# Performance work log

Measured on AMD Instinct MI355X. Metric: run time of the kernel, lower is better.

Reference implementation:

```python
import jax, jax.numpy as jnp
import numpy as np

N, E, F_IN, HID, HEADS, CLASSES = 50000, 800000, 128, 128, 4, 2
NEG_SLOPE = 0.2


def _gatv2_layer(x, Wl, Wr, att, bias, src, dst, heads, concat):
    # PyG GATv2Conv (share_weights=False, eval mode):
    #   e_ij = att . leaky_relu(Wl x_j + Wr x_i); alpha = segment_softmax over dst;
    #   out_i = sum_j alpha_ij * (Wl x_j)
    n = x.shape[0]
    c = att.shape[-1]
    xl = (x @ Wl).reshape(n, heads, c)   # source transform [N,H,C]
    xr = (x @ Wr).reshape(n, heads, c)   # target transform [N,H,C]
    e = jax.nn.leaky_relu(xl[src] + xr[dst], NEG_SLOPE)      # [E,H,C]
    logits = jnp.einsum('ehc,hc->eh', e, att)                # [E,H]
    m = jax.ops.segment_max(logits, dst, num_segments=n)     # stable softmax per dst
    p = jnp.exp(logits - m[dst])
    denom = jax.ops.segment_sum(p, dst, num_segments=n)
    alpha = p / (denom[dst] + 1e-16)                         # [E,H]
    out = jax.ops.segment_sum(alpha[:, :, None] * xl[src], dst, num_segments=n)  # [N,H,C]
    out = out.reshape(n, heads * c) if concat else out.mean(axis=1)
    return out + bias


def setup_inputs() -> dict:
    key = jax.random.key(0)
    ks = jax.random.split(key, 16)
    s = lambda fan_in: 1.0 / np.sqrt(fan_in)
    inp = {
        'x': jax.random.normal(ks[0], (N, F_IN), jnp.float32),
        'edge_idx': jax.random.randint(ks[1], (2, E), 0, N, jnp.int64),
        'w_in': jax.random.normal(ks[2], (F_IN, HID), jnp.float32) * s(F_IN),
        'b_in': jnp.zeros((HID,), jnp.float32),
        'wl1': jax.random.normal(ks[3], (HID, HEADS * HID), jnp.float32) * s(HID),
        'wr1': jax.random.normal(ks[4], (HID, HEADS * HID), jnp.float32) * s(HID),
        'att1': jax.random.normal(ks[5], (HEADS, HID), jnp.float32) * s(HID),
        'b1': jnp.zeros((HEADS * HID,), jnp.float32),
        'wl2': jax.random.normal(ks[6], (HEADS * HID, HID), jnp.float32) * s(HEADS * HID),
        'wr2': jax.random.normal(ks[7], (HEADS * HID, HID), jnp.float32) * s(HEADS * HID),
        'att2': jax.random.normal(ks[8], (1, HID), jnp.float32) * s(HID),
        'b2': jnp.zeros((HID,), jnp.float32),
        'w_out': jax.random.normal(ks[9], (HID, CLASSES), jnp.float32) * s(HID),
        'b_out': jnp.zeros((CLASSES,), jnp.float32),
    }
    return inp


def reference(x, edge_idx, w_in, b_in, wl1, wr1, att1, b1, wl2, wr2, att2, b2, w_out, b_out):
    n = x.shape[0]
    loops = jnp.arange(n, dtype=edge_idx.dtype)  # PyG add_self_loops=True
    src = jnp.concatenate([edge_idx[0], loops])
    dst = jnp.concatenate([edge_idx[1], loops])
    h = jax.nn.elu(x @ w_in + b_in)              # dropout is identity in eval
    h = jax.nn.elu(_gatv2_layer(h, wl1, wr1, att1, b1, src, dst, HEADS, True))
    h = jax.nn.elu(_gatv2_layer(h, wl2, wr2, att2, b2, src, dst, 1, False))
    logits = h @ w_out + b_out
    return jax.nn.log_softmax(logits, axis=1)
```

## Files before the change

kernel.cpp:

```cpp
#include <hip/hip_runtime.h>
#include <hip/hip_bf16.h>
#include <math.h>

#define F_IN   128
#define HID    128
#define HEADS  4
#define HC1    (HEADS*HID)
#define CLASSES 2
#define NEG_SLOPE 0.2f

#define SCAN_CHUNK 2048

typedef __attribute__((ext_vector_type(8))) short short8;
typedef __attribute__((ext_vector_type(4))) float f32x4;

__global__ void zero_int_kernel(int* __restrict__ p, int n) {
    int i = blockIdx.x * blockDim.x + threadIdx.x;
    int stride = gridDim.x * blockDim.x;
    for (; i < n; i += stride) p[i] = 0;
}

__global__ void deg_kernel(const int* __restrict__ dst_arr, int* __restrict__ deg,
                           int E, int N) {
    int e = blockIdx.x * blockDim.x + threadIdx.x;
    if (e >= E) return;
    int d = dst_arr[e];
    if ((unsigned)d >= (unsigned)N) d = 0;
    atomicAdd(&deg[d], 1);
}

__global__ void scan_partial_kernel(const int* __restrict__ deg, int* __restrict__ bsum, int n) {
    __shared__ int sdata[256];
    int b = blockIdx.x, t = threadIdx.x;
    int base = b * SCAN_CHUNK;
    int s = 0;
    for (int i = t; i < SCAN_CHUNK; i += 256) {
        int idx = base + i;
        s += (idx < n) ? deg[idx] : 0;
    }
    sdata[t] = s;
    __syncthreads();
    for (int off = 128; off; off >>= 1) {
        if (t < off) sdata[t] += sdata[t + off];
        __syncthreads();
    }
    if (t == 0) bsum[b] = sdata[0];
}

__global__ void scan_bsums_kernel(int* __restrict__ bsum, int nb, int* __restrict__ row, int n) {
    if (blockIdx.x == 0 && threadIdx.x == 0) {
        int acc = 0;
        for (int i = 0; i < nb; ++i) { int v = bsum[i]; bsum[i] = acc; acc += v; }
        row[n] = acc;
    }
}

__global__ void scan_final_kernel(const int* __restrict__ deg, const int* __restrict__ bsum,
                                  int* __restrict__ row, int* __restrict__ cursor, int n) {
    __shared__ int tsum[256];
    int b = blockIdx.x, t = threadIdx.x;
    int base = b * SCAN_CHUNK + t * 8;
    int local[8];
    int s = 0;
    #pragma unroll
    for (int k = 0; k < 8; ++k) {
        int idx = base + k;
        int v = (idx < n) ? deg[idx] : 0;
        local[k] = s;
        s += v;
    }
    tsum[t] = s;
    __syncthreads();
    for (int off = 1; off < 256; off <<= 1) {
        int v = 0;
        if (t >= off) v = tsum[t - off];
        __syncthreads();
        if (t >= off) tsum[t] += v;
        __syncthreads();
    }
    int texcl = (t == 0) ? 0 : tsum[t - 1];
    int boff = bsum[b];
    #pragma unroll
    for (int k = 0; k < 8; ++k) {
        int idx = base + k;
        if (idx < n) {
            int v = boff + texcl + local[k];
            row[idx] = v;
            cursor[idx] = v;
        }
    }
}

__global__ void scatter_kernel(const int* __restrict__ src_arr, const int* __restrict__ dst_arr,
                               int* __restrict__ cursor, int* __restrict__ src_sorted,
                               int E, int N) {
    int e = blockIdx.x * blockDim.x + threadIdx.x;
    if (e >= E) return;
    int s = src_arr[e], d = dst_arr[e];
    if ((unsigned)s >= (unsigned)N) s = 0;
    if ((unsigned)d >= (unsigned)N) d = 0;
    int pos = atomicAdd(&cursor[d], 1);
    src_sorted[pos] = s;
}

__global__ void transpose_to_bf16_kernel(const float* __restrict__ w,
                                         __hip_bfloat16* __restrict__ wT,
                                         int K, int N) {
    int t = blockIdx.x * blockDim.x + threadIdx.x;
    if (t >= K * N) return;
    int n = t / K, k = t % K;
    wT[t] = __float2bfloat16(w[(size_t)k * N + n]);
}

__global__ void f32_to_bf16_kernel(const float* __restrict__ in,
                                   __hip_bfloat16* __restrict__ outb, int n) {
    int i = blockIdx.x * blockDim.x + threadIdx.x;
    int stride = gridDim.x * blockDim.x;
    short* ob = (short*)outb;
    for (int base = i * 4; base < n; base += stride * 4) {
        float4 v = *(const float4*)(in + base);
        __hip_bfloat16 h0 = __float2bfloat16(v.x);
        __hip_bfloat16 h1 = __float2bfloat16(v.y);
        __hip_bfloat16 h2 = __float2bfloat16(v.z);
        __hip_bfloat16 h3 = __float2bfloat16(v.w);
        short4 sv;
        sv.x = *reinterpret_cast<short*>(&h0);
        sv.y = *reinterpret_cast<short*>(&h1);
        sv.z = *reinterpret_cast<short*>(&h2);
        sv.w = *reinterpret_cast<short*>(&h3);
        *(short4*)(ob + base) = sv;
    }
}

template<int ACT, typename OutT>
__global__ __launch_bounds__(256) void gemm_kernel(
    const float* __restrict__ A, const float* __restrict__ B,
    const float* __restrict__ bias, OutT* __restrict__ C,
    int M, int K, int N)
{
    const int tx = threadIdx.x & 15;
    const int ty = threadIdx.x >> 4;
    const int row0 = blockIdx.y * 64;
    const int col0 = blockIdx.x * 64;

    __shared__ float As[16][68];
    __shared__ float Bs[16][68];

    float acc[4][4] = {};

    for (int k0 = 0; k0 < K; k0 += 16) {
        #pragma unroll
        for (int idx = threadIdx.x; idx < 64 * 16; idx += 256) {
            int r = idx >> 4, c = idx & 15;
            int gr = row0 + r;
            float v = (gr < M) ? A[(size_t)gr * K + (k0 + c)] : 0.0f;
            As[c][r] = v;
        }
        #pragma unroll
        for (int idx = threadIdx.x; idx < 16 * 64; idx += 256) {
            int r = idx >> 6, c = idx & 63;
            Bs[r][c] = B[(size_t)(k0 + r) * N + (col0 + c)];
        }
        __syncthreads();
        #pragma unroll
        for (int k = 0; k < 16; ++k) {
            float a[4], b[4];
            #pragma unroll
            for (int i = 0; i < 4; ++i) a[i] = As[k][ty * 4 + i];
            #pragma unroll
            for (int j = 0; j < 4; ++j) b[j] = Bs[k][tx * 4 + j];
            #pragma unroll
            for (int i = 0; i < 4; ++i)
                #pragma unroll
                for (int j = 0; j < 4; ++j)
                    acc[i][j] += a[i] * b[j];
        }
        __syncthreads();
    }

    #pragma unroll
    for (int i = 0; i < 4; ++i) {
        int r = row0 + ty * 4 + i;
        if (r >= M) continue;
        #pragma unroll
        for (int j = 0; j < 4; ++j) {
            int c = col0 + tx * 4 + j;
            float v = acc[i][j] + (bias ? bias[c] : 0.0f);
            if (ACT == 1) v = (v > 0.0f) ? v : expm1f(v);
            C[(size_t)r * N + c] = (OutT)v;
        }
    }
}

template<typename OutT>
__global__ __launch_bounds__(256) void mfma_gemm_kernel(
    const __hip_bfloat16* __restrict__ A,
    const __hip_bfloat16* __restrict__ BT,
    OutT* __restrict__ C,
    int M, int K, int N)
{
    constexpr int BM = 128, BN = 64, BK = 64, LDA = 72;
    __shared__ __align__(16) short As[BM * LDA];
    __shared__ __align__(16) short Bs[BN * LDA];

    const int tid  = threadIdx.x;
    const int lane = tid & 63;
    const int wid  = tid >> 6;
    const int wm   = wid >> 1;
    const int wn   = wid & 1;
    const int fr   = lane & 15;
    const int fk   = (lane >> 4) * 8;

    const int row0 = blockIdx.y * BM;
    const int col0 = blockIdx.x * BN;

    const short* Ag = (const short*)A;
    const short* Bg = (const short*)BT;

    f32x4 acc[4][2] = {};

    for (int k0 = 0; k0 < K; k0 += BK) {
        #pragma unroll
        for (int it = 0; it < 4; ++it) {
            int chunk = it * 256 + tid;
            int r = chunk >> 3, c = chunk & 7;
            int gr = row0 + r;
            short8 v = {0, 0, 0, 0, 0, 0, 0, 0};
            if (gr < M) v = *(const short8*)(Ag + (size_t)gr * K + k0 + c * 8);
            *(short8*)(&As[r * LDA + c * 8]) = v;
        }
        #pragma unroll
        for (int it = 0; it < 2; ++it) {
            int chunk = it * 256 + tid;
            int n = chunk >> 3, c = chunk & 7;
            short8 v = *(const short8*)(Bg + (size_t)(col0 + n) * K + k0 + c * 8);
            *(short8*)(&Bs[n * LDA + c * 8]) = v;
        }
        __syncthreads();
        #pragma unroll
        for (int kk = 0; kk < 2; ++kk) {
            short8 af[4], bf[2];
            #pragma unroll
            for (int i = 0; i < 4; ++i)
                af[i] = *(const short8*)(&As[(wm * 64 + i * 16 + fr) * LDA + kk * 32 + fk]);
            #pragma unroll
            for (int j = 0; j < 2; ++j)
                bf[j] = *(const short8*)(&Bs[(wn * 32 + j * 16 + fr) * LDA + kk * 32 + fk]);
            #pragma unroll
            for (int i = 0; i < 4; ++i)
                #pragma unroll
                for (int j = 0; j < 2; ++j)
                    acc[i][j] = __builtin_amdgcn_mfma_f32_16x16x32_bf16(af[i], bf[j], acc[i][j], 0, 0, 0);
        }
        __syncthreads();
    }

    const int crow = row0 + wm * 64;
    const int ccol = col0 + wn * 32;
    #pragma unroll
    for (int i = 0; i < 4; ++i) {
        #pragma unroll
        for (int j = 0; j < 2; ++j) {
            int col = ccol + j * 16 + (lane & 15);
            #pragma unroll
            for (int reg = 0; reg < 4; ++reg) {
                int r = crow + i * 16 + (lane >> 4) * 4 + reg;
                if (r < M) C[(size_t)r * N + col] = (OutT)acc[i][j][reg];
            }
        }
    }
}

__global__ __launch_bounds__(256) void gatv2_l1_fused_kernel(
    const __hip_bfloat16* __restrict__ xl, const __hip_bfloat16* __restrict__ xr,
    const int* __restrict__ row, const int* __restrict__ src_sorted,
    const float* __restrict__ att, const float* __restrict__ b1,
    __hip_bfloat16* __restrict__ out1, int N)
{
    int d = blockIdx.x * 4 + (threadIdx.x >> 6);
    if (d >= N) return;
    int lane = threadIdx.x & 63;
    int cbase = lane * 8;

    float xrd[8], attv[8];
    {
        uint4 raw = *reinterpret_cast<const uint4*>(xr + (size_t)d * HC1 + cbase);
        const unsigned* u = reinterpret_cast<const unsigned*>(&raw);
        #pragma unroll
        for (int j = 0; j < 4; ++j) {
            xrd[2 * j]     = __uint_as_float(u[j] << 16);
            xrd[2 * j + 1] = __uint_as_float(u[j] & 0xffff0000u);
        }
        #pragma unroll
        for (int k = 0; k < 8; ++k) attv[k] = att[cbase + k];
    }

    float m = -__builtin_huge_valf();
    float s = 0.0f;
    float o[8] = {};

    int rs = row[d], re = row[d + 1];

    for (int it = rs - 1; it < re; ++it) {
        int srcn = (it < rs) ? d : src_sorted[it];
        float v[8];
        uint4 raw = *reinterpret_cast<const uint4*>(xl + (size_t)srcn * HC1 + cbase);
        const unsigned* u = reinterpret_cast<const unsigned*>(&raw);
        #pragma unroll
        for (int j = 0; j < 4; ++j) {
            v[2 * j]     = __uint_as_float(u[j] << 16);
            v[2 * j + 1] = __uint_as_float(u[j] & 0xffff0000u);
        }
        float t = 0.0f;
        #pragma unroll
        for (int k = 0; k < 8; ++k) {
            float e = v[k] + xrd[k];
            e = (e > 0.0f) ? e : NEG_SLOPE * e;
            t = fmaf(e, attv[k], t);
        }
        t += __shfl_xor(t, 1);
        t += __shfl_xor(t, 2);
        t += __shfl_xor(t, 4);
        t += __shfl_xor(t, 8);
        if (t > m) {
            float r = __expf(m - t);
            s *= r;
            #pragma unroll
            for (int k = 0; k < 8; ++k) o[k] *= r;
            m = t;
        }
        float p = __expf(t - m);
        s += p;
        #pragma unroll
        for (int k = 0; k < 8; ++k) o[k] = fmaf(p, v[k], o[k]);
    }

    float inv = 1.0f / (s + 1e-16f);
    short8 sv;
    #pragma unroll
    for (int k = 0; k < 8; ++k) {
        float val = o[k] * inv + b1[cbase + k];
        val = (val > 0.0f) ? val : expm1f(val);
        __hip_bfloat16 hb = __float2bfloat16(val);
        sv[k] = *reinterpret_cast<short*>(&hb);
    }
    *(short8*)((short*)out1 + (size_t)d * HC1 + cbase) = sv;
}

__global__ __launch_bounds__(256) void gatv2_l2_final_kernel(
    const float* __restrict__ xl2, const float* __restrict__ xr2,
    const int* __restrict__ row, const int* __restrict__ src_sorted,
    const float* __restrict__ att2, const float* __restrict__ b2,
    const float* __restrict__ w_out, const float* __restrict__ b_out,
    float* __restrict__ out, int N)
{
    int d = blockIdx.x * 4 + (threadIdx.x >> 6);
    if (d >= N) return;
    int lane = threadIdx.x & 63;
    int c0 = lane * 2;

    float2 xrd  = *reinterpret_cast<const float2*>(xr2 + (size_t)d * HID + c0);
    float2 attv = *reinterpret_cast<const float2*>(att2 + c0);

    float m = -__builtin_huge_valf();
    float s = 0.0f;
    float o0 = 0.0f, o1 = 0.0f;

    int rs = row[d], re = row[d + 1];
    for (int it = rs - 1; it < re; ++it) {
        int srcn = (it < rs) ? d : src_sorted[it];
        float2 v = *reinterpret_cast<const float2*>(xl2 + (size_t)srcn * HID + c0);
        float e0 = v.x + xrd.x; e0 = (e0 > 0.0f) ? e0 : NEG_SLOPE * e0;
        float e1 = v.y + xrd.y; e1 = (e1 > 0.0f) ? e1 : NEG_SLOPE * e1;
        float t = fmaf(e0, attv.x, e1 * attv.y);
        #pragma unroll
        for (int off = 32; off; off >>= 1) t += __shfl_xor(t, off);
        if (t > m) {
            float r = __expf(m - t);
            s *= r; o0 *= r; o1 *= r;
            m = t;
        }
        float p = __expf(t - m);
        s += p;
        o0 = fmaf(p, v.x, o0);
        o1 = fmaf(p, v.y, o1);
    }

    float inv = 1.0f / (s + 1e-16f);
    float h0v = o0 * inv + b2[c0];
    float h1v = o1 * inv + b2[c0 + 1];
    h0v = (h0v > 0.0f) ? h0v : expm1f(h0v);
    h1v = (h1v > 0.0f) ? h1v : expm1f(h1v);

    float a0 = fmaf(h0v, w_out[c0 * 2 + 0], h1v * w_out[(c0 + 1) * 2 + 0]);
    float a1 = fmaf(h0v, w_out[c0 * 2 + 1], h1v * w_out[(c0 + 1) * 2 + 1]);
    #pragma unroll
    for (int off = 32; off; off >>= 1) {
        a0 += __shfl_xor(a0, off);
        a1 += __shfl_xor(a1, off);
    }
    if (lane == 0) {
        float z0 = a0 + b_out[0];
        float z1 = a1 + b_out[1];
        float mx = fmaxf(z0, z1);
        float lse = mx + logf(__expf(z0 - mx) + __expf(z1 - mx));
        out[(size_t)d * CLASSES + 0] = z0 - lse;
        out[(size_t)d * CLASSES + 1] = z1 - lse;
    }
}

extern "C" void kernel_launch(void* const* d_in, const int* in_sizes, int n_in,
                              void* d_out, int out_size, void* d_ws, size_t ws_size,
                              hipStream_t stream)
{
    const float* x     = (const float*)d_in[0];
    const int*   eidx  = (const int*)d_in[1];
    const float* w_in  = (const float*)d_in[2];
    const float* b_in  = (const float*)d_in[3];
    const float* wl1   = (const float*)d_in[4];
    const float* wr1   = (const float*)d_in[5];
    const float* att1  = (const float*)d_in[6];
    const float* b1    = (const float*)d_in[7];
    const float* wl2   = (const float*)d_in[8];
    const float* wr2   = (const float*)d_in[9];
    const float* att2  = (const float*)d_in[10];
    const float* b2    = (const float*)d_in[11];
    const float* w_out = (const float*)d_in[12];
    const float* b_out = (const float*)d_in[13];
    float* out = (float*)d_out;

    const int N = in_sizes[0] / F_IN;
    const int E = in_sizes[1] / 2;
    const int* src_arr = eidx;
    const int* dst_arr = eidx + E;

    size_t off = 0;
    auto alloc = [&](size_t bytes) -> char* {
        char* ptr = (char*)d_ws + off;
        off += (bytes + 255) & ~(size_t)255;
        return ptr;
    };
    int* row        = (int*)alloc((size_t)(N + 1) * 4);
    int* cursor     = (int*)alloc((size_t)N * 4);
    int* deg        = (int*)alloc((size_t)N * 4);
    int* bsum       = (int*)alloc(64 * 4);
    int* src_sorted = (int*)alloc((size_t)E * 4);
    __hip_bfloat16* wT1l = (__hip_bfloat16*)alloc((size_t)HID * HC1 * 2);
    __hip_bfloat16* wT1r = (__hip_bfloat16*)alloc((size_t)HID * HC1 * 2);
    __hip_bfloat16* wT2l = (__hip_bfloat16*)alloc((size_t)HC1 * HID * 2);
    __hip_bfloat16* wT2r = (__hip_bfloat16*)alloc((size_t)HC1 * HID * 2);
    float*          h0   = (float*)alloc((size_t)N * HID * 4);
    __hip_bfloat16* h0b  = (__hip_bfloat16*)alloc((size_t)N * HID * 2);
    __hip_bfloat16* xl1  = (__hip_bfloat16*)alloc((size_t)N * HC1 * 2);
    __hip_bfloat16* xr1  = (__hip_bfloat16*)alloc((size_t)N * HC1 * 2);
    __hip_bfloat16* out1 = (__hip_bfloat16*)alloc((size_t)N * HC1 * 2);

    float* xl2 = h0;
    float* xr2 = (float*)xl1;

    dim3 blk(256);
    const int NB_SCAN = (N + SCAN_CHUNK - 1) / SCAN_CHUNK;

    hipLaunchKernelGGL(zero_int_kernel, dim3(64), blk, 0, stream, deg, N);
    hipLaunchKernelGGL(deg_kernel, dim3((E + 255) / 256), blk, 0, stream, dst_arr, deg, E, N);
    hipLaunchKernelGGL(scan_partial_kernel, dim3(NB_SCAN), blk, 0, stream, deg, bsum, N);
    hipLaunchKernelGGL(scan_bsums_kernel, dim3(1), blk, 0, stream, bsum, NB_SCAN, row, N);
    hipLaunchKernelGGL(scan_final_kernel, dim3(NB_SCAN), blk, 0, stream, deg, bsum, row, cursor, N);
    hipLaunchKernelGGL(scatter_kernel, dim3((E + 255) / 256), blk, 0, stream,
                       src_arr, dst_arr, cursor, src_sorted, E, N);

    {
        dim3 gw((HID * HC1 + 255) / 256);
        hipLaunchKernelGGL(transpose_to_bf16_kernel, gw, blk, 0, stream, wl1, wT1l, HID, HC1);
        hipLaunchKernelGGL(transpose_to_bf16_kernel, gw, blk, 0, stream, wr1, wT1r, HID, HC1);
        hipLaunchKernelGGL(transpose_to_bf16_kernel, gw, blk, 0, stream, wl2, wT2l, HC1, HID);
        hipLaunchKernelGGL(transpose_to_bf16_kernel, gw, blk, 0, stream, wr2, wT2r, HC1, HID);
    }

    {
        dim3 grid(HID / 64, (N + 63) / 64);
        hipLaunchKernelGGL((gemm_kernel<1, float>), grid, blk, 0, stream,
                           x, w_in, b_in, h0, N, F_IN, HID);
        hipLaunchKernelGGL(f32_to_bf16_kernel, dim3(2048), blk, 0, stream, h0, h0b, N * HID);
    }
    {
        dim3 grid(HC1 / 64, (N + 127) / 128);
        hipLaunchKernelGGL((mfma_gemm_kernel<__hip_bfloat16>), grid, blk, 0, stream,
                           h0b, wT1l, xl1, N, HID, HC1);
        hipLaunchKernelGGL((mfma_gemm_kernel<__hip_bfloat16>), grid, blk, 0, stream,
                           h0b, wT1r, xr1, N, HID, HC1);
    }
    {
        dim3 grid((N + 3) / 4);
        hipLaunchKernelGGL(gatv2_l1_fused_kernel, grid, blk, 0, stream,
                           xl1, xr1, row, src_sorted, att1, b1, out1, N);
    }
    {
        dim3 grid(HID / 64, (N + 127) / 128);
        hipLaunchKernelGGL((mfma_gemm_kernel<float>), grid, blk, 0, stream,
                           out1, wT2l, xl2, N, HC1, HID);
        hipLaunchKernelGGL((mfma_gemm_kernel<float>), grid, blk, 0, stream,
                           out1, wT2r, xr2, N, HC1, HID);
    }
    {
        dim3 grid((N + 3) / 4);
        hipLaunchKernelGGL(gatv2_l2_final_kernel, grid, blk, 0, stream,
                           xl2, xr2, row, src_sorted, att2, b2, w_out, b_out, out, N);
    }
}
```

Before: 647.2 us.

## Merge Wl/Wr GEMMs into one, use MFMA for input layer, prefetch gathers

Concatenates the left and right weight matrices so each GAT layer needs a single MFMA GEMM writing an interleaved [xl|xr] bf16 row per node. The input projection moves from the scalar fp32 GEMM to the bf16 MFMA GEMM with fused bias and ELU, and layer-2 features are stored in bf16 instead of fp32, halving gather traffic. Both attention kernels software-prefetch the next neighbour's row to hide gather latency. The cost is lower precision in the input layer and the layer-2 features, and a wider row stride for the gathers.

```diff
diff --git a/kernel.cpp b/kernel.cpp
--- a/kernel.cpp
+++ b/kernel.cpp
@@ -133,69 +133,10 @@
 }
 
 template<int ACT, typename OutT>
-__global__ __launch_bounds__(256) void gemm_kernel(
-    const float* __restrict__ A, const float* __restrict__ B,
-    const float* __restrict__ bias, OutT* __restrict__ C,
-    int M, int K, int N)
-{
-    const int tx = threadIdx.x & 15;
-    const int ty = threadIdx.x >> 4;
-    const int row0 = blockIdx.y * 64;
-    const int col0 = blockIdx.x * 64;
-
-    __shared__ float As[16][68];
-    __shared__ float Bs[16][68];
-
-    float acc[4][4] = {};
-
-    for (int k0 = 0; k0 < K; k0 += 16) {
-        #pragma unroll
-        for (int idx = threadIdx.x; idx < 64 * 16; idx += 256) {
-            int r = idx >> 4, c = idx & 15;
-            int gr = row0 + r;
-            float v = (gr < M) ? A[(size_t)gr * K + (k0 + c)] : 0.0f;
-            As[c][r] = v;
-        }
-        #pragma unroll
-        for (int idx = threadIdx.x; idx < 16 * 64; idx += 256) {
-            int r = idx >> 6, c = idx & 63;
-            Bs[r][c] = B[(size_t)(k0 + r) * N + (col0 + c)];
-        }
-        __syncthreads();
-        #pragma unroll
-        for (int k = 0; k < 16; ++k) {
-            float a[4], b[4];
-            #pragma unroll
-            for (int i = 0; i < 4; ++i) a[i] = As[k][ty * 4 + i];
-            #pragma unroll
-            for (int j = 0; j < 4; ++j) b[j] = Bs[k][tx * 4 + j];
-            #pragma unroll
-            for (int i = 0; i < 4; ++i)
-                #pragma unroll
-                for (int j = 0; j < 4; ++j)
-                    acc[i][j] += a[i] * b[j];
-        }
-        __syncthreads();
-    }
-
-    #pragma unroll
-    for (int i = 0; i < 4; ++i) {
-        int r = row0 + ty * 4 + i;
-        if (r >= M) continue;
-        #pragma unroll
-        for (int j = 0; j < 4; ++j) {
-            int c = col0 + tx * 4 + j;
-            float v = acc[i][j] + (bias ? bias[c] : 0.0f);
-            if (ACT == 1) v = (v > 0.0f) ? v : expm1f(v);
-            C[(size_t)r * N + c] = (OutT)v;
-        }
-    }
-}
-
-template<typename OutT>
 __global__ __launch_bounds__(256) void mfma_gemm_kernel(
     const __hip_bfloat16* __restrict__ A,
     const __hip_bfloat16* __restrict__ BT,
+    const float* __restrict__ bias,
     OutT* __restrict__ C,
     int M, int K, int N)
 {
@@ -262,17 +203,22 @@
         #pragma unroll
         for (int j = 0; j < 2; ++j) {
             int col = ccol + j * 16 + (lane & 15);
+            float bv = bias ? bias[col] : 0.0f;
             #pragma unroll
             for (int reg = 0; reg < 4; ++reg) {
                 int r = crow + i * 16 + (lane >> 4) * 4 + reg;
-                if (r < M) C[(size_t)r * N + col] = (OutT)acc[i][j][reg];
+                if (r < M) {
+                    float v = acc[i][j][reg] + bv;
+                    if (ACT == 1) v = (v > 0.0f) ? v : expm1f(v);
+                    C[(size_t)r * N + col] = (OutT)v;
+                }
             }
         }
     }
 }
 
 __global__ __launch_bounds__(256) void gatv2_l1_fused_kernel(
-    const __hip_bfloat16* __restrict__ xl, const __hip_bfloat16* __restrict__ xr,
+    const __hip_bfloat16* __restrict__ xlr,
     const int* __restrict__ row, const int* __restrict__ src_sorted,
     const float* __restrict__ att, const float* __restrict__ b1,
     __hip_bfloat16* __restrict__ out1, int N)
@@ -281,10 +227,11 @@
     if (d >= N) return;
     int lane = threadIdx.x & 63;
     int cbase = lane * 8;
+    const short* base = (const short*)xlr;
 
     float xrd[8], attv[8];
     {
-        uint4 raw = *reinterpret_cast<const uint4*>(xr + (size_t)d * HC1 + cbase);
+        uint4 raw = *reinterpret_cast<const uint4*>(base + (size_t)d * 1024 + 512 + cbase);
         const unsigned* u = reinterpret_cast<const unsigned*>(&raw);
         #pragma unroll
         for (int j = 0; j < 4; ++j) {
@@ -301,11 +248,15 @@
 
     int rs = row[d], re = row[d + 1];
 
+    uint4 raw = *reinterpret_cast<const uint4*>(base + (size_t)d * 1024 + cbase);
     for (int it = rs - 1; it < re; ++it) {
-        int srcn = (it < rs) ? d : src_sorted[it];
+        uint4 cur = raw;
+        if (it + 1 < re) {
+            int sn = src_sorted[it + 1];
+            raw = *reinterpret_cast<const uint4*>(base + (size_t)sn * 1024 + cbase);
+        }
         float v[8];
-        uint4 raw = *reinterpret_cast<const uint4*>(xl + (size_t)srcn * HC1 + cbase);
-        const unsigned* u = reinterpret_cast<const unsigned*>(&raw);
+        const unsigned* u = reinterpret_cast<const unsigned*>(&cur);
         #pragma unroll
         for (int j = 0; j < 4; ++j) {
             v[2 * j]     = __uint_as_float(u[j] << 16);
@@ -348,7 +299,7 @@
 }
 
 __global__ __launch_bounds__(256) void gatv2_l2_final_kernel(
-    const float* __restrict__ xl2, const float* __restrict__ xr2,
+    const __hip_bfloat16* __restrict__ xlr2,
     const int* __restrict__ row, const int* __restrict__ src_sorted,
     const float* __restrict__ att2, const float* __restrict__ b2,
     const float* __restrict__ w_out, const float* __restrict__ b_out,
@@ -358,8 +309,11 @@
     if (d >= N) return;
     int lane = threadIdx.x & 63;
     int c0 = lane * 2;
-
-    float2 xrd  = *reinterpret_cast<const float2*>(xr2 + (size_t)d * HID + c0);
+    const short* base = (const short*)xlr2;
+
+    unsigned xr_raw = *reinterpret_cast<const unsigned*>(base + (size_t)d * 256 + 128 + c0);
+    float xrd0 = __uint_as_float(xr_raw << 16);
+    float xrd1 = __uint_as_float(xr_raw & 0xffff0000u);
     float2 attv = *reinterpret_cast<const float2*>(att2 + c0);
 
     float m = -__builtin_huge_valf();
@@ -367,11 +321,17 @@
     float o0 = 0.0f, o1 = 0.0f;
 
     int rs = row[d], re = row[d + 1];
+    unsigned raw = *reinterpret_cast<const unsigned*>(base + (size_t)d * 256 + c0);
     for (int it = rs - 1; it < re; ++it) {
-        int srcn = (it < rs) ? d : src_sorted[it];
-        float2 v = *reinterpret_cast<const float2*>(xl2 + (size_t)srcn * HID + c0);
-        float e0 = v.x + xrd.x; e0 = (e0 > 0.0f) ? e0 : NEG_SLOPE * e0;
-        float e1 = v.y + xrd.y; e1 = (e1 > 0.0f) ? e1 : NEG_SLOPE * e1;
+        unsigned cur = raw;
+        if (it + 1 < re) {
+            int sn = src_sorted[it + 1];
+            raw = *reinterpret_cast<const unsigned*>(base + (size_t)sn * 256 + c0);
+        }
+        float v0 = __uint_as_float(cur << 16);
+        float v1 = __uint_as_float(cur & 0xffff0000u);
+        float e0 = v0 + xrd0; e0 = (e0 > 0.0f) ? e0 : NEG_SLOPE * e0;
+        float e1 = v1 + xrd1; e1 = (e1 > 0.0f) ? e1 : NEG_SLOPE * e1;
         float t = fmaf(e0, attv.x, e1 * attv.y);
         #pragma unroll
         for (int off = 32; off; off >>= 1) t += __shfl_xor(t, off);
@@ -382,8 +342,8 @@
         }
         float p = __expf(t - m);
         s += p;
-        o0 = fmaf(p, v.x, o0);
-        o1 = fmaf(p, v.y, o1);
+        o0 = fmaf(p, v0, o0);
+        o1 = fmaf(p, v1, o1);
     }
 
     float inv = 1.0f / (s + 1e-16f);
@@ -445,18 +405,15 @@
     int* deg        = (int*)alloc((size_t)N * 4);
     int* bsum       = (int*)alloc(64 * 4);
     int* src_sorted = (int*)alloc((size_t)E * 4);
-    __hip_bfloat16* wT1l = (__hip_bfloat16*)alloc((size_t)HID * HC1 * 2);
-    __hip_bfloat16* wT1r = (__hip_bfloat16*)alloc((size_t)HID * HC1 * 2);
-    __hip_bfloat16* wT2l = (__hip_bfloat16*)alloc((size_t)HC1 * HID * 2);
-    __hip_bfloat16* wT2r = (__hip_bfloat16*)alloc((size_t)HC1 * HID * 2);
-    float*          h0   = (float*)alloc((size_t)N * HID * 4);
-    __hip_bfloat16* h0b  = (__hip_bfloat16*)alloc((size_t)N * HID * 2);
-    __hip_bfloat16* xl1  = (__hip_bfloat16*)alloc((size_t)N * HC1 * 2);
-    __hip_bfloat16* xr1  = (__hip_bfloat16*)alloc((size_t)N * HC1 * 2);
-    __hip_bfloat16* out1 = (__hip_bfloat16*)alloc((size_t)N * HC1 * 2);
-
-    float* xl2 = h0;
-    float* xr2 = (float*)xl1;
+    __hip_bfloat16* w_inT = (__hip_bfloat16*)alloc((size_t)F_IN * HID * 2);
+    __hip_bfloat16* wT1   = (__hip_bfloat16*)alloc((size_t)2 * HC1 * HID * 2);
+    __hip_bfloat16* wT2   = (__hip_bfloat16*)alloc((size_t)2 * HID * HC1 * 2);
+    __hip_bfloat16* xb    = (__hip_bfloat16*)alloc((size_t)N * F_IN * 2);
+    __hip_bfloat16* h0b   = (__hip_bfloat16*)alloc((size_t)N * HID * 2);
+    __hip_bfloat16* xlr1  = (__hip_bfloat16*)alloc((size_t)N * 2 * HC1 * 2);
+    __hip_bfloat16* out1  = (__hip_bfloat16*)alloc((size_t)N * HC1 * 2);
+
+    __hip_bfloat16* xlr2 = xlr1;
 
     dim3 blk(256);
     const int NB_SCAN = (N + SCAN_CHUNK - 1) / SCAN_CHUNK;
@@ -471,40 +428,38 @@
 
     {
         dim3 gw((HID * HC1 + 255) / 256);
-        hipLaunchKernelGGL(transpose_to_bf16_kernel, gw, blk, 0, stream, wl1, wT1l, HID, HC1);
-        hipLaunchKernelGGL(transpose_to_bf16_kernel, gw, blk, 0, stream, wr1, wT1r, HID, HC1);
-        hipLaunchKernelGGL(transpose_to_bf16_kernel, gw, blk, 0, stream, wl2, wT2l, HC1, HID);
-        hipLaunchKernelGGL(transpose_to_bf16_kernel, gw, blk, 0, stream, wr2, wT2r, HC1, HID);
-    }
-
-    {
-        dim3 grid(HID / 64, (N + 63) / 64);
-        hipLaunchKernelGGL((gemm_kernel<1, float>), grid, blk, 0, stream,
-                           x, w_in, b_in, h0, N, F_IN, HID);
-        hipLaunchKernelGGL(f32_to_bf16_kernel, dim3(2048), blk, 0, stream, h0, h0b, N * HID);
-    }
-    {
-        dim3 grid(HC1 / 64, (N + 127) / 128);
-        hipLaunchKernelGGL((mfma_gemm_kernel<__hip_bfloat16>), grid, blk, 0, stream,
-                           h0b, wT1l, xl1, N, HID, HC1);
-        hipLaunchKernelGGL((mfma_gemm_kernel<__hip_bfloat16>), grid, blk, 0, stream,
-                           h0b, wT1r, xr1, N, HID, HC1);
+        dim3 gwi((F_IN * HID + 255) / 256);
+        hipLaunchKernelGGL(transpose_to_bf16_kernel, gwi, blk, 0, stream, w_in, w_inT, F_IN, HID);
+        hipLaunchKernelGGL(transpose_to_bf16_kernel, gw, blk, 0, stream, wl1, wT1, HID, HC1);
+        hipLaunchKernelGGL(transpose_to_bf16_kernel, gw, blk, 0, stream, wr1, wT1 + (size_t)HC1 * HID, HID, HC1);
+        hipLaunchKernelGGL(transpose_to_bf16_kernel, gw, blk, 0, stream, wl2, wT2, HC1, HID);
+        hipLaunchKernelGGL(transpose_to_bf16_kernel, gw, blk, 0, stream, wr2, wT2 + (size_t)HID * HC1, HC1, HID);
+    }
+
+    hipLaunchKernelGGL(f32_to_bf16_kernel, dim3(2048), blk, 0, stream, x, xb, N * F_IN);
+    {
+        dim3 grid(HID / 64, (N + 127) / 128);
+        hipLaunchKernelGGL((mfma_gemm_kernel<1, __hip_bfloat16>), grid, blk, 0, stream,
+                           xb, w_inT, b_in, h0b, N, F_IN, HID);
+    }
+    {
+        dim3 grid(2 * HC1 / 64, (N + 127) / 128);
+        hipLaunchKernelGGL((mfma_gemm_kernel<0, __hip_bfloat16>), grid, blk, 0, stream,
+                           h0b, wT1, (const float*)nullptr, xlr1, N, HID, 2 * HC1);
     }
     {
         dim3 grid((N + 3) / 4);
         hipLaunchKernelGGL(gatv2_l1_fused_kernel, grid, blk, 0, stream,
-                           xl1, xr1, row, src_sorted, att1, b1, out1, N);
-    }
-    {
-        dim3 grid(HID / 64, (N + 127) / 128);
-        hipLaunchKernelGGL((mfma_gemm_kernel<float>), grid, blk, 0, stream,
-                           out1, wT2l, xl2, N, HC1, HID);
-        hipLaunchKernelGGL((mfma_gemm_kernel<float>), grid, blk, 0, stream,
-                           out1, wT2r, xr2, N, HC1, HID);
+                           xlr1, row, src_sorted, att1, b1, out1, N);
+    }
+    {
+        dim3 grid(2 * HID / 64, (N + 127) / 128);
+        hipLaunchKernelGGL((mfma_gemm_kernel<0, __hip_bfloat16>), grid, blk, 0, stream,
+                           out1, wT2, (const float*)nullptr, xlr2, N, HC1, 2 * HID);
     }
     {
         dim3 grid((N + 3) / 4);
         hipLaunchKernelGGL(gatv2_l2_final_kernel, grid, blk, 0, stream,
-                           xl2, xr2, row, src_sorted, att2, b2, w_out, b_out, out, N);
-    }
-}
+                           xlr2, row, src_sorted, att2, b2, w_out, b_out, out, N);
+    }
+}
```

Result: faster. 603.2 us (-6.8%).
